# Kernel optimization log

Measured on AMD Instinct MI355X. Metric: run time of the kernel, lower is better.

The kernel has to match this reference:

```python
import jax, jax.numpy as jnp
import numpy as np


def setup_inputs() -> dict:
    key = jax.random.key(0)
    k1, k2 = jax.random.split(key)
    T, D, K = 100000, 768, 500  # frames, feature dim (HuBERT base), k-means clusters
    feat = jax.random.normal(k1, (T, D), dtype=jnp.float32)
    C = jax.random.normal(k2, (D, K), dtype=jnp.float32)  # cluster centers, transposed as in module
    return {"feat": feat, "C": C}


def reference(feat, C):
    # Squared euclidean distance expanded: ||f||^2 - 2 f.C + ||c||^2
    Cnorm = jnp.sum(C * C, axis=0, keepdims=True)            # [1, K]
    fnorm = jnp.sum(feat * feat, axis=1, keepdims=True)       # [T, 1]
    dist = fnorm - 2.0 * jnp.matmul(feat, C) + Cnorm          # [T, K]
    return jnp.argmin(dist, axis=1)[None, :]                  # [1, T] cluster ids
```

## Files before the change

### kernel.cpp

```cpp
#include <hip/hip_runtime.h>
#include <float.h>

#define D_DIM 768
#define K_DIM 500
#define NDT   24
#define BM    64
#define NTH   256
#define PB_STRIDE 100352

typedef _Float16 f16x8 __attribute__((ext_vector_type(8)));
typedef float    f32x4 __attribute__((ext_vector_type(4)));


__global__ void cnorm_partial_kernel(const float* __restrict__ C,
                                     double* __restrict__ partial, int K) {
    const int k = threadIdx.x;
    const int w = blockIdx.x;
    double s = 0.0;
    if (k < K) {
        const int d0 = w * (D_DIM / 16);
        for (int d = d0; d < d0 + (D_DIM / 16); ++d) {
            const float c = C[(size_t)d * K + k];
            s = fma((double)c, (double)c, s);
        }
    }
    partial[w * 512 + k] = s;
}

__global__ void cnorm_finish_kernel(const double* __restrict__ partial,
                                    float* __restrict__ cnorm, int K) {
    const int k = threadIdx.x;
    if (k < K) {
        double s = 0.0;
        for (int w = 0; w < 16; ++w) s += partial[w * 512 + k];
        cnorm[k] = (float)s;
    } else {
        cnorm[k] = FLT_MAX;
    }
}

__global__ void packB_kernel(const float* __restrict__ C,
                             _Float16* __restrict__ BpH,
                             _Float16* __restrict__ BpL) {
    const int idx = blockIdx.x * 256 + threadIdx.x;
    const int col = idx & 511;
    const int dt  = idx >> 9;
    f16x8 h[4], l[4];
    #pragma unroll
    for (int c = 0; c < 4; ++c)
        #pragma unroll
        for (int j = 0; j < 8; ++j) {
            const int k = c * 8 + j;
            const float v = (col < K_DIM)
                          ? C[(size_t)(dt * 32 + k) * K_DIM + col] : 0.0f;
            const _Float16 hh = (_Float16)v;
            h[c][j] = hh;
            l[c][j] = (_Float16)(v - (float)hh);
        }
    f16x8* dH = (f16x8*)(BpH + ((size_t)dt * 512 + col) * 32);
    f16x8* dL = (f16x8*)(BpL + ((size_t)dt * 512 + col) * 32);
    #pragma unroll
    for (int c = 0; c < 4; ++c) { dH[c] = h[c]; dL[c] = l[c]; }
}

__launch_bounds__(NTH, 3)
__global__ void assign_kernel(const float* __restrict__ feat,
                              const _Float16* __restrict__ BpH,
                              const _Float16* __restrict__ BpL,
                              const float* __restrict__ cnorm,
                              float* __restrict__ pbv,
                              int* __restrict__ pbi,
                              int T) {
    __shared__ __align__(16) _Float16 AsH[2][BM * 32];
    __shared__ __align__(16) _Float16 AsL[2][BM * 32];
    __shared__ float red_v[BM * 4];
    __shared__ int   red_i[BM * 4];

    const int tid  = threadIdx.x;
    const int wn   = tid >> 6;
    const int lane = tid & 63;
    const int l15  = lane & 15;
    const int kg   = lane >> 4;
    const int bid  = blockIdx.x;
    const int half = bid & 1;
    const int R0   = (bid >> 1) * BM;

    const int ar = tid >> 2;
    const int ac = (tid & 3) << 3;
    const bool arow_ok = (R0 + ar) < T;
    const float* fptr = feat + (size_t)(R0 + ar) * D_DIM + ac;
    const int asl = ((ac >> 3) + (ar >> 1)) & 3;

    const int colbase = half * 256 + wn * 64 + l15;
    const _Float16* bpH = BpH + (size_t)colbase * 32 + kg * 8;
    const _Float16* bpL = BpL + (size_t)colbase * 32 + kg * 8;

    f32x4 acc[4][4];
    #pragma unroll
    for (int m = 0; m < 4; ++m)
        #pragma unroll
        for (int n = 0; n < 4; ++n) acc[m][n] = (f32x4){0.f, 0.f, 0.f, 0.f};

    {
        float4 v0 = make_float4(0.f, 0.f, 0.f, 0.f), v1 = v0;
        if (arow_ok) {
            v0 = *(const float4*)(fptr);
            v1 = *(const float4*)(fptr + 4);
        }
        const float fa[8] = {v0.x, v0.y, v0.z, v0.w, v1.x, v1.y, v1.z, v1.w};
        f16x8 h, l;
        #pragma unroll
        for (int j = 0; j < 8; ++j) {
            const _Float16 hh = (_Float16)fa[j];
            h[j] = hh; l[j] = (_Float16)(fa[j] - (float)hh);
        }
        ((f16x8*)AsH[0])[ar * 4 + asl] = h;
        ((f16x8*)AsL[0])[ar * 4 + asl] = l;
    }
    __syncthreads();

    for (int dt = 0; dt < NDT; ++dt) {
        const int cur = dt & 1;
        const bool hasNext = (dt + 1) < NDT;

        f16x8 aH[4], aL[4];
        #pragma unroll
        for (int m = 0; m < 4; ++m) {
            const int row = m * 16 + l15;
            const int sl  = (kg + (row >> 1)) & 3;
            aH[m] = ((const f16x8*)AsH[cur])[row * 4 + sl];
            aL[m] = ((const f16x8*)AsL[cur])[row * 4 + sl];
        }

        const size_t bo = (size_t)dt * 16384;
        f16x8 bH[4], bL[4];
        #pragma unroll
        for (int nh = 0; nh < 4; ++nh) {
            bH[nh] = *(const f16x8*)(bpH + bo + nh * 512);
            bL[nh] = *(const f16x8*)(bpL + bo + nh * 512);
        }

        float4 v0 = make_float4(0.f, 0.f, 0.f, 0.f), v1 = v0;
        if (hasNext && arow_ok) {
            v0 = *(const float4*)(fptr + (dt + 1) * 32);
            v1 = *(const float4*)(fptr + (dt + 1) * 32 + 4);
        }

        #pragma unroll
        for (int nh = 0; nh < 4; ++nh) {
            #pragma unroll
            for (int m = 0; m < 4; ++m) {
                f32x4 a = acc[m][nh];
                a = __builtin_amdgcn_mfma_f32_16x16x32_f16(aH[m], bH[nh], a, 0, 0, 0);
                a = __builtin_amdgcn_mfma_f32_16x16x32_f16(aL[m], bH[nh], a, 0, 0, 0);
                a = __builtin_amdgcn_mfma_f32_16x16x32_f16(aH[m], bL[nh], a, 0, 0, 0);
                acc[m][nh] = a;
            }
        }

        if (hasNext) {
            const float fa[8] = {v0.x, v0.y, v0.z, v0.w, v1.x, v1.y, v1.z, v1.w};
            f16x8 h, l;
            #pragma unroll
            for (int j = 0; j < 8; ++j) {
                const _Float16 hh = (_Float16)fa[j];
                h[j] = hh; l[j] = (_Float16)(fa[j] - (float)hh);
            }
            ((f16x8*)AsH[cur ^ 1])[ar * 4 + asl] = h;
            ((f16x8*)AsL[cur ^ 1])[ar * 4 + asl] = l;
        }
        __syncthreads();
    }

    float cn[4];
    #pragma unroll
    for (int nh = 0; nh < 4; ++nh)
        cn[nh] = cnorm[half * 256 + wn * 64 + nh * 16 + l15];

    #pragma unroll
    for (int m = 0; m < 4; ++m) {
        #pragma unroll
        for (int r = 0; r < 4; ++r) {
            float best = cn[0] - 2.0f * acc[m][0][r];
            int   bi   = colbase;
            #pragma unroll
            for (int nh = 1; nh < 4; ++nh) {
                const int col = colbase + nh * 16;
                const float s = cn[nh] - 2.0f * acc[m][nh][r];
                if (s < best || (s == best && col < bi)) { best = s; bi = col; }
            }
            #pragma unroll
            for (int msk = 1; msk < 16; msk <<= 1) {
                const float ov = __shfl_xor(best, msk, 64);
                const int   oi = __shfl_xor(bi,   msk, 64);
                if (ov < best || (ov == best && oi < bi)) { best = ov; bi = oi; }
            }
            if (l15 == 0) {
                const int rl = m * 16 + kg * 4 + r;
                red_v[rl * 4 + wn] = best;
                red_i[rl * 4 + wn] = bi;
            }
        }
    }
    __syncthreads();

    if (tid < BM) {
        float bv = red_v[tid * 4];
        int   bi = red_i[tid * 4];
        #pragma unroll
        for (int w = 1; w < 4; ++w) {
            const float v = red_v[tid * 4 + w];
            const int   i = red_i[tid * 4 + w];
            if (v < bv || (v == bv && i < bi)) { bv = v; bi = i; }
        }
        const int r = R0 + tid;
        if (r < T) {
            pbv[(size_t)half * PB_STRIDE + r] = bv;
            pbi[(size_t)half * PB_STRIDE + r] = bi;
        }
    }
}

__global__ void combine_kernel(const float* __restrict__ pbv,
                               const int* __restrict__ pbi,
                               int* __restrict__ out, int T) {
    const int r = blockIdx.x * 256 + threadIdx.x;
    if (r < T) {
        const float s0 = pbv[r];
        const int   i0 = pbi[r];
        const float s1 = pbv[PB_STRIDE + r];
        const int   i1 = pbi[PB_STRIDE + r];
        out[r] = (s1 < s0) ? i1 : i0;
    }
}

extern "C" void kernel_launch(void* const* d_in, const int* in_sizes, int n_in,
                              void* d_out, int out_size, void* d_ws, size_t ws_size,
                              hipStream_t stream) {
    const float* feat = (const float*)d_in[0];
    const float* C    = (const float*)d_in[1];
    int* out          = (int*)d_out;
    const int T = in_sizes[0] / D_DIM;
    const int K = in_sizes[1] / D_DIM;

    float*     cnorm   = (float*)d_ws;
    double*    partial = (double*)((char*)d_ws + 4096);
    _Float16*  BpH     = (_Float16*)((char*)d_ws + 131072);
    _Float16*  BpL     = (_Float16*)((char*)d_ws + 917504);
    float*     pbv     = (float*)((char*)d_ws + 1703936);
    int*       pbi     = (int*)((char*)d_ws + 2506752);

    hipLaunchKernelGGL(cnorm_partial_kernel, dim3(16), dim3(512), 0, stream,
                       C, partial, K);
    hipLaunchKernelGGL(cnorm_finish_kernel, dim3(1), dim3(512), 0, stream,
                       partial, cnorm, K);
    hipLaunchKernelGGL(packB_kernel, dim3(48), dim3(256), 0, stream,
                       C, BpH, BpL);

    const int nrb = (T + BM - 1) / BM;
    hipLaunchKernelGGL(assign_kernel, dim3(nrb * 2), dim3(NTH), 0, stream,
                       feat, BpH, BpL, cnorm, pbv, pbi, T);
    hipLaunchKernelGGL(combine_kernel, dim3((T + 255) / 256), dim3(256), 0, stream,
                       pbv, pbi, out, T);
}
```

Before: 272.2 us.

## Load feature rows directly into registers, dropping shared-memory A staging and barriers

Each wave now reads its own 64 feature rows straight from global memory into registers and splits them into fp16 hi/lo there, instead of staging them through double-buffered LDS with a __syncthreads per k-step. This removes the LDS traffic and block-wide barriers. The cost is that all four waves redundantly load and convert the same A rows, four times the global/L2 reads and conversion ALU work, and there is no explicit prefetch. The MFMA section is also wrapped in s_setprio to raise wave priority.

```diff
diff --git a/kernel.cpp b/kernel.cpp
--- a/kernel.cpp
+++ b/kernel.cpp
@@ -71,8 +71,6 @@
                               float* __restrict__ pbv,
                               int* __restrict__ pbi,
                               int T) {
-    __shared__ __align__(16) _Float16 AsH[2][BM * 32];
-    __shared__ __align__(16) _Float16 AsL[2][BM * 32];
     __shared__ float red_v[BM * 4];
     __shared__ int   red_i[BM * 4];
 
@@ -85,11 +83,14 @@
     const int half = bid & 1;
     const int R0   = (bid >> 1) * BM;
 
-    const int ar = tid >> 2;
-    const int ac = (tid & 3) << 3;
-    const bool arow_ok = (R0 + ar) < T;
-    const float* fptr = feat + (size_t)(R0 + ar) * D_DIM + ac;
-    const int asl = ((ac >> 3) + (ar >> 1)) & 3;
+    int r0 = R0 +  0 + l15; r0 = r0 < T ? r0 : T - 1;
+    int r1 = R0 + 16 + l15; r1 = r1 < T ? r1 : T - 1;
+    int r2 = R0 + 32 + l15; r2 = r2 < T ? r2 : T - 1;
+    int r3 = R0 + 48 + l15; r3 = r3 < T ? r3 : T - 1;
+    const float* ap0 = feat + (size_t)r0 * D_DIM + kg * 8;
+    const float* ap1 = feat + (size_t)r1 * D_DIM + kg * 8;
+    const float* ap2 = feat + (size_t)r2 * D_DIM + kg * 8;
+    const float* ap3 = feat + (size_t)r3 * D_DIM + kg * 8;
 
     const int colbase = half * 256 + wn * 64 + l15;
     const _Float16* bpH = BpH + (size_t)colbase * 32 + kg * 8;
@@ -101,36 +102,28 @@
         #pragma unroll
         for (int n = 0; n < 4; ++n) acc[m][n] = (f32x4){0.f, 0.f, 0.f, 0.f};
 
-    {
-        float4 v0 = make_float4(0.f, 0.f, 0.f, 0.f), v1 = v0;
-        if (arow_ok) {
-            v0 = *(const float4*)(fptr);
-            v1 = *(const float4*)(fptr + 4);
-        }
-        const float fa[8] = {v0.x, v0.y, v0.z, v0.w, v1.x, v1.y, v1.z, v1.w};
-        f16x8 h, l;
-        #pragma unroll
-        for (int j = 0; j < 8; ++j) {
-            const _Float16 hh = (_Float16)fa[j];
-            h[j] = hh; l[j] = (_Float16)(fa[j] - (float)hh);
-        }
-        ((f16x8*)AsH[0])[ar * 4 + asl] = h;
-        ((f16x8*)AsL[0])[ar * 4 + asl] = l;
-    }
-    __syncthreads();
-
+#define SPLIT8(V0, V1, H, L) do {                                              \
+    const float fa_[8] = {(V0).x, (V0).y, (V0).z, (V0).w,                      \
+                          (V1).x, (V1).y, (V1).z, (V1).w};                     \
+    _Pragma("unroll")                                                          \
+    for (int j = 0; j < 8; ++j) {                                              \
+        const _Float16 hh = (_Float16)fa_[j];                                  \
+        (H)[j] = hh; (L)[j] = (_Float16)(fa_[j] - (float)hh);                  \
+    }                                                                          \
+} while (0)
+
+    #pragma unroll 1
     for (int dt = 0; dt < NDT; ++dt) {
-        const int cur = dt & 1;
-        const bool hasNext = (dt + 1) < NDT;
-
-        f16x8 aH[4], aL[4];
-        #pragma unroll
-        for (int m = 0; m < 4; ++m) {
-            const int row = m * 16 + l15;
-            const int sl  = (kg + (row >> 1)) & 3;
-            aH[m] = ((const f16x8*)AsH[cur])[row * 4 + sl];
-            aL[m] = ((const f16x8*)AsL[cur])[row * 4 + sl];
-        }
+        const int o = dt * 32;
+
+        const float4 a00 = *(const float4*)(ap0 + o);
+        const float4 a01 = *(const float4*)(ap0 + o + 4);
+        const float4 a10 = *(const float4*)(ap1 + o);
+        const float4 a11 = *(const float4*)(ap1 + o + 4);
+        const float4 a20 = *(const float4*)(ap2 + o);
+        const float4 a21 = *(const float4*)(ap2 + o + 4);
+        const float4 a30 = *(const float4*)(ap3 + o);
+        const float4 a31 = *(const float4*)(ap3 + o + 4);
 
         const size_t bo = (size_t)dt * 16384;
         f16x8 bH[4], bL[4];
@@ -140,14 +133,15 @@
             bL[nh] = *(const f16x8*)(bpL + bo + nh * 512);
         }
 
-        float4 v0 = make_float4(0.f, 0.f, 0.f, 0.f), v1 = v0;
-        if (hasNext && arow_ok) {
-            v0 = *(const float4*)(fptr + (dt + 1) * 32);
-            v1 = *(const float4*)(fptr + (dt + 1) * 32 + 4);
-        }
-
-        #pragma unroll
-        for (int nh = 0; nh < 4; ++nh) {
+        f16x8 aH[4], aL[4];
+        SPLIT8(a00, a01, aH[0], aL[0]);
+        SPLIT8(a10, a11, aH[1], aL[1]);
+        SPLIT8(a20, a21, aH[2], aL[2]);
+        SPLIT8(a30, a31, aH[3], aL[3]);
+
+        __builtin_amdgcn_s_setprio(1);
+        #pragma unroll
+        for (int nh = 0; nh < 4; ++nh)
             #pragma unroll
             for (int m = 0; m < 4; ++m) {
                 f32x4 a = acc[m][nh];
@@ -156,21 +150,9 @@
                 a = __builtin_amdgcn_mfma_f32_16x16x32_f16(aH[m], bL[nh], a, 0, 0, 0);
                 acc[m][nh] = a;
             }
-        }
-
-        if (hasNext) {
-            const float fa[8] = {v0.x, v0.y, v0.z, v0.w, v1.x, v1.y, v1.z, v1.w};
-            f16x8 h, l;
-            #pragma unroll
-            for (int j = 0; j < 8; ++j) {
-                const _Float16 hh = (_Float16)fa[j];
-                h[j] = hh; l[j] = (_Float16)(fa[j] - (float)hh);
-            }
-            ((f16x8*)AsH[cur ^ 1])[ar * 4 + asl] = h;
-            ((f16x8*)AsL[cur ^ 1])[ar * 4 + asl] = l;
-        }
-        __syncthreads();
-    }
+        __builtin_amdgcn_s_setprio(0);
+    }
+#undef SPLIT8
 
     float cn[4];
     #pragma unroll
```

Measured after the change: 456.7 us. 1.68x slower.

## Raise assign kernel occupancy, split A fragment loads, use lighter barrier

Applied to the files above, without the earlier changes.

Raises launch bounds from 3 to 4 waves per SIMD and loads the A fragments in two groups of two rows instead of all four, which lowers live VGPRs. MFMA blocks are wrapped in s_setprio, the main loop is kept rolled, and __syncthreads is replaced by an LDS-only waitcnt plus s_barrier. BpL is reached through a fixed offset from BpH, which removes one pointer. The tighter register budget may cause spills, and the lighter barrier relies on global loads not needing to drain before the barrier.

```diff
diff --git a/kernel.cpp b/kernel.cpp
--- a/kernel.cpp
+++ b/kernel.cpp
@@ -7,6 +7,7 @@
 #define BM    64
 #define NTH   256
 #define PB_STRIDE 100352
+#define BLOFF 393216
 
 typedef _Float16 f16x8 __attribute__((ext_vector_type(8)));
 typedef float    f32x4 __attribute__((ext_vector_type(4)));
@@ -63,10 +64,9 @@
     for (int c = 0; c < 4; ++c) { dH[c] = h[c]; dL[c] = l[c]; }
 }
 
-__launch_bounds__(NTH, 3)
+__launch_bounds__(NTH, 4)
 __global__ void assign_kernel(const float* __restrict__ feat,
                               const _Float16* __restrict__ BpH,
-                              const _Float16* __restrict__ BpL,
                               const float* __restrict__ cnorm,
                               float* __restrict__ pbv,
                               int* __restrict__ pbi,
@@ -91,15 +91,31 @@
     const float* fptr = feat + (size_t)(R0 + ar) * D_DIM + ac;
     const int asl = ((ac >> 3) + (ar >> 1)) & 3;
 
-    const int colbase = half * 256 + wn * 64 + l15;
-    const _Float16* bpH = BpH + (size_t)colbase * 32 + kg * 8;
-    const _Float16* bpL = BpL + (size_t)colbase * 32 + kg * 8;
+    const _Float16* bp = BpH + (size_t)(half * 256 + wn * 64 + l15) * 32 + kg * 8;
 
     f32x4 acc[4][4];
     #pragma unroll
     for (int m = 0; m < 4; ++m)
         #pragma unroll
         for (int n = 0; n < 4; ++n) acc[m][n] = (f32x4){0.f, 0.f, 0.f, 0.f};
+
+#define CVT_STORE(V0, V1, BUF) do {                                            \
+    const float fa[8] = {(V0).x, (V0).y, (V0).z, (V0).w,                       \
+                         (V1).x, (V1).y, (V1).z, (V1).w};                      \
+    f16x8 h, l;                                                                \
+    _Pragma("unroll")                                                          \
+    for (int j = 0; j < 8; ++j) {                                              \
+        const _Float16 hh = (_Float16)fa[j];                                   \
+        h[j] = hh; l[j] = (_Float16)(fa[j] - (float)hh);                       \
+    }                                                                          \
+    ((f16x8*)AsH[BUF])[ar * 4 + asl] = h;                                      \
+    ((f16x8*)AsL[BUF])[ar * 4 + asl] = l;                                      \
+} while (0)
+
+#define SOFT_BARRIER() do {                                                    \
+    asm volatile("s_waitcnt lgkmcnt(0)" ::: "memory");                         \
+    __builtin_amdgcn_s_barrier();                                              \
+} while (0)
 
     {
         float4 v0 = make_float4(0.f, 0.f, 0.f, 0.f), v1 = v0;
@@ -107,37 +123,21 @@
             v0 = *(const float4*)(fptr);
             v1 = *(const float4*)(fptr + 4);
         }
-        const float fa[8] = {v0.x, v0.y, v0.z, v0.w, v1.x, v1.y, v1.z, v1.w};
-        f16x8 h, l;
-        #pragma unroll
-        for (int j = 0; j < 8; ++j) {
-            const _Float16 hh = (_Float16)fa[j];
-            h[j] = hh; l[j] = (_Float16)(fa[j] - (float)hh);
-        }
-        ((f16x8*)AsH[0])[ar * 4 + asl] = h;
-        ((f16x8*)AsL[0])[ar * 4 + asl] = l;
+        CVT_STORE(v0, v1, 0);
     }
     __syncthreads();
 
+    #pragma unroll 1
     for (int dt = 0; dt < NDT; ++dt) {
         const int cur = dt & 1;
         const bool hasNext = (dt + 1) < NDT;
 
-        f16x8 aH[4], aL[4];
-        #pragma unroll
-        for (int m = 0; m < 4; ++m) {
-            const int row = m * 16 + l15;
-            const int sl  = (kg + (row >> 1)) & 3;
-            aH[m] = ((const f16x8*)AsH[cur])[row * 4 + sl];
-            aL[m] = ((const f16x8*)AsL[cur])[row * 4 + sl];
-        }
-
         const size_t bo = (size_t)dt * 16384;
         f16x8 bH[4], bL[4];
         #pragma unroll
         for (int nh = 0; nh < 4; ++nh) {
-            bH[nh] = *(const f16x8*)(bpH + bo + nh * 512);
-            bL[nh] = *(const f16x8*)(bpL + bo + nh * 512);
+            bH[nh] = *(const f16x8*)(bp + bo + nh * 512);
+            bL[nh] = *(const f16x8*)(bp + BLOFF + bo + nh * 512);
         }
 
         float4 v0 = make_float4(0.f, 0.f, 0.f, 0.f), v1 = v0;
@@ -147,35 +147,44 @@
         }
 
         #pragma unroll
-        for (int nh = 0; nh < 4; ++nh) {
-            #pragma unroll
-            for (int m = 0; m < 4; ++m) {
-                f32x4 a = acc[m][nh];
-                a = __builtin_amdgcn_mfma_f32_16x16x32_f16(aH[m], bH[nh], a, 0, 0, 0);
-                a = __builtin_amdgcn_mfma_f32_16x16x32_f16(aL[m], bH[nh], a, 0, 0, 0);
-                a = __builtin_amdgcn_mfma_f32_16x16x32_f16(aH[m], bL[nh], a, 0, 0, 0);
-                acc[m][nh] = a;
-            }
+        for (int mg = 0; mg < 2; ++mg) {
+            f16x8 aH[2], aL[2];
+            #pragma unroll
+            for (int mm = 0; mm < 2; ++mm) {
+                const int row = (mg * 2 + mm) * 16 + l15;
+                const int sl  = (kg + (row >> 1)) & 3;
+                aH[mm] = ((const f16x8*)AsH[cur])[row * 4 + sl];
+                aL[mm] = ((const f16x8*)AsL[cur])[row * 4 + sl];
+            }
+            __builtin_amdgcn_s_setprio(1);
+            #pragma unroll
+            for (int mm = 0; mm < 2; ++mm) {
+                const int m = mg * 2 + mm;
+                #pragma unroll
+                for (int nh = 0; nh < 4; ++nh) {
+                    f32x4 a = acc[m][nh];
+                    a = __builtin_amdgcn_mfma_f32_16x16x32_f16(aH[mm], bH[nh], a, 0, 0, 0);
+                    a = __builtin_amdgcn_mfma_f32_16x16x32_f16(aL[mm], bH[nh], a, 0, 0, 0);
+                    a = __builtin_amdgcn_mfma_f32_16x16x32_f16(aH[mm], bL[nh], a, 0, 0, 0);
+                    acc[m][nh] = a;
+                }
+            }
+            __builtin_amdgcn_s_setprio(0);
         }
 
         if (hasNext) {
-            const float fa[8] = {v0.x, v0.y, v0.z, v0.w, v1.x, v1.y, v1.z, v1.w};
-            f16x8 h, l;
-            #pragma unroll
-            for (int j = 0; j < 8; ++j) {
-                const _Float16 hh = (_Float16)fa[j];
-                h[j] = hh; l[j] = (_Float16)(fa[j] - (float)hh);
-            }
-            ((f16x8*)AsH[cur ^ 1])[ar * 4 + asl] = h;
-            ((f16x8*)AsL[cur ^ 1])[ar * 4 + asl] = l;
-        }
-        __syncthreads();
-    }
-
+            CVT_STORE(v0, v1, cur ^ 1);
+        }
+        SOFT_BARRIER();
+    }
+#undef SOFT_BARRIER
+#undef CVT_STORE
+
+    const int colbase = half * 256 + wn * 64 + l15;
     float cn[4];
     #pragma unroll
     for (int nh = 0; nh < 4; ++nh)
-        cn[nh] = cnorm[half * 256 + wn * 64 + nh * 16 + l15];
+        cn[nh] = cnorm[colbase + nh * 16];
 
     #pragma unroll
     for (int m = 0; m < 4; ++m) {
@@ -259,7 +268,7 @@
 
     const int nrb = (T + BM - 1) / BM;
     hipLaunchKernelGGL(assign_kernel, dim3(nrb * 2), dim3(NTH), 0, stream,
-                       feat, BpH, BpL, cnorm, pbv, pbi, T);
+                       feat, BpH, cnorm, pbv, pbi, T);
     hipLaunchKernelGGL(combine_kernel, dim3((T + 255) / 256), dim3(256), 0, stream,
                        pbv, pbi, out, T);
 }
```

Measured after the change: 266.2 us. 2.2% less time.
